# Kernel tuning notes

Measured on AMD Instinct MI355X. Metric: run time of the kernel, lower is better.

The kernel has to match this reference:

```python
import jax, jax.numpy as jnp
import numpy as np

N_HEADS = 16  # emb_dim 512 // head_dim 32


def _heads(t, h=N_HEADS):
    b, n, d = t.shape
    return t.reshape(b, n, h, d // h).transpose(0, 2, 1, 3)  # [b h n hd]


def _merge(t):
    b, h, n, hd = t.shape
    return t.transpose(0, 2, 1, 3).reshape(b, n, h * hd)


def setup_inputs() -> dict:
    key = jax.random.key(0)
    ks = jax.random.split(key, 6)
    b, n, nc, d = 2, 2048, 256, 512
    x = jax.random.normal(ks[0], (b, n, d), dtype=jnp.float32)
    clusters = jax.random.normal(ks[1], (b, nc, d), dtype=jnp.float32)
    token_sizes = jax.random.uniform(ks[2], (b, n), dtype=jnp.float32)
    Wq = jax.random.normal(ks[3], (d, d), dtype=jnp.float32) * 0.02
    Wkv = jax.random.normal(ks[4], (d, 2 * d), dtype=jnp.float32) * 0.02
    Wo = jax.random.normal(ks[5], (d, d), dtype=jnp.float32) * 0.02
    return {"x": x, "clusters": clusters, "token_sizes": token_sizes,
            "Wq": Wq, "Wkv": Wkv, "Wo": Wo}


def reference(x, clusters, token_sizes, Wq, Wkv, Wo):
    b, n, d = x.shape
    hd = d // N_HEADS
    scale = hd ** -0.5

    q_in = jnp.concatenate([x, clusters], axis=1)       # pack tokens + clusters as queries
    q = _heads(q_in @ Wq)                               # [b h n+nc hd]
    kv = x @ Wkv                                        # [b n 2d]
    k = _heads(kv[..., :d])                             # [b h n hd]
    v = _heads(kv[..., d:])                             # [b h n hd]

    attn = jnp.einsum('bhqd,bhkd->bhqk', q, k) * scale  # [b h n+nc n]
    attn_x = attn[:, :, :n, :]                          # token queries  [b h n n]
    attn_c = attn[:, :, n:, :]                          # cluster queries [b h nc n]

    # soft assignment: softmax over cluster axis, then row-normalize
    a_c = jax.nn.softmax(attn_c, axis=-2)
    a_c = a_c / (jnp.sum(a_c, axis=-1, keepdims=True) + 1e-5)
    clusters_out = _merge(jnp.einsum('bhck,bhkd->bhcd', a_c, v)) @ Wo  # [b nc d]

    # additive log token-size bias on the query axis (as in the original)
    attn_x = attn_x + jnp.log(token_sizes + 1e-10)[:, None, :, None]
    a_x = jax.nn.softmax(attn_x, axis=-1)
    x_out = _merge(jnp.einsum('bhqk,bhkd->bhqd', a_x, v)) @ Wo  # [b n d]

    return x_out, clusters_out
```

## Files before the change

kernel.cpp:

```cpp
#include <hip/hip_runtime.h>
#include <hip/hip_bf16.h>

#define N_TOK 2048
#define N_CLU 256
#define N_ALL 2304
#define DMODEL 512
#define NH 16
#define HD 32
#define BATCH 2
#define SCALE 0.17677669529663687f

typedef short bf16x8 __attribute__((ext_vector_type(8)));
typedef float f32x4  __attribute__((ext_vector_type(4)));
typedef unsigned short u16;

static __device__ __forceinline__ u16 f2b(float x) {
    __hip_bfloat16 h = __float2bfloat16(x);
    return *reinterpret_cast<u16*>(&h);
}
static __device__ __forceinline__ unsigned int cvt_pk_bf16(float lo, float hi) {
    unsigned int r;
    asm("v_cvt_pk_bf16_f32 %0, %1, %2" : "=v"(r) : "v"(lo), "v"(hi));
    return r;
}
static __device__ __forceinline__ void async16(u16* lds, const u16* g) {
    __builtin_amdgcn_global_load_lds(
        (const __attribute__((address_space(1))) unsigned int*)g,
        (__attribute__((address_space(3))) unsigned int*)lds, 16, 0, 0);
}

__global__ __launch_bounds__(256) void cvt_bf16_k(const float* __restrict__ in,
                                                  u16* __restrict__ out)
{
    const long i = ((long)blockIdx.x * 256 + threadIdx.x) * 8;
    float4 a = *(const float4*)(in + i);
    float4 b = *(const float4*)(in + i + 4);
    u16 v[8] = { f2b(a.x), f2b(a.y), f2b(a.z), f2b(a.w),
                 f2b(b.x), f2b(b.y), f2b(b.z), f2b(b.w) };
    *(bf16x8*)(out + i) = *(const bf16x8*)v;
}

__global__ __launch_bounds__(256) void cvtT_k(const float* __restrict__ W,
                                              u16* __restrict__ WT,
                                              int R, int C, float scale)
{
    __shared__ float tile[32][33];
    const int tx = threadIdx.x & 31, ty = threadIdx.x >> 5;
    const int c0 = blockIdx.x * 32, r0 = blockIdx.y * 32;
    #pragma unroll
    for (int i = 0; i < 4; i++)
        tile[ty + i * 8][tx] = W[(long)(r0 + ty + i * 8) * C + c0 + tx];
    __syncthreads();
    #pragma unroll
    for (int i = 0; i < 4; i++)
        WT[(long)(c0 + ty + i * 8) * R + r0 + tx] = f2b(tile[tx][ty + i * 8] * scale);
}

__global__ __launch_bounds__(256) void gemm_bf16(
    const u16* __restrict__ A, long sA,
    const u16* __restrict__ BT,
    void* __restrict__ Cv, long sC,
    int N, int K, int out_fp32)
{
    const int t = threadIdx.x;
    const int m0 = blockIdx.y * 128, n0 = blockIdx.x * 128;
    A += (long)blockIdx.z * sA;
    __shared__ u16 As[128 * 32];
    __shared__ u16 Bs[128 * 32];
    const int wid = t >> 6, lane = t & 63;
    const int lr = lane & 15, lg = lane >> 4;
    const int wr = wid >> 1, wc = wid & 1;
    f32x4 acc[4][4] = {};
    const int o1 = t * 16, o2 = o1 + 4096;
    const int row1 = o1 >> 6, ke1 = (o1 & 63) >> 1;
    const int row2 = o2 >> 6, ke2 = (o2 & 63) >> 1;
    for (int k0 = 0; k0 < K; k0 += 32) {
        async16(As + (o1 >> 1), A  + (long)(m0 + row1) * K + k0 + ke1);
        async16(As + (o2 >> 1), A  + (long)(m0 + row2) * K + k0 + ke2);
        async16(Bs + (o1 >> 1), BT + (long)(n0 + row1) * K + k0 + ke1);
        async16(Bs + (o2 >> 1), BT + (long)(n0 + row2) * K + k0 + ke2);
        __syncthreads();
        bf16x8 af[4], bfr[4];
        #pragma unroll
        for (int i = 0; i < 4; i++) {
            af[i]  = *(const bf16x8*)&As[(wr * 64 + i * 16 + lr) * 32 + lg * 8];
            bfr[i] = *(const bf16x8*)&Bs[(wc * 64 + i * 16 + lr) * 32 + lg * 8];
        }
        #pragma unroll
        for (int mi = 0; mi < 4; mi++)
            #pragma unroll
            for (int ni = 0; ni < 4; ni++)
                acc[mi][ni] = __builtin_amdgcn_mfma_f32_16x16x32_bf16(af[mi], bfr[ni], acc[mi][ni], 0, 0, 0);
        __syncthreads();
    }
    if (out_fp32) {
        float* C = (float*)Cv + (long)blockIdx.z * sC;
        #pragma unroll
        for (int mi = 0; mi < 4; mi++)
            #pragma unroll
            for (int ni = 0; ni < 4; ni++) {
                const long rbase = m0 + wr * 64 + mi * 16 + lg * 4;
                #pragma unroll
                for (int r = 0; r < 4; r++)
                    C[(rbase + r) * N + n0 + wc * 64 + ni * 16 + lr] = acc[mi][ni][r];
            }
    } else {
        u16* C = (u16*)Cv + (long)blockIdx.z * sC;
        #pragma unroll
        for (int mi = 0; mi < 4; mi++)
            #pragma unroll
            for (int ni = 0; ni < 4; ni++) {
                const long rbase = m0 + wr * 64 + mi * 16 + lg * 4;
                #pragma unroll
                for (int r = 0; r < 4; r++)
                    C[(rbase + r) * N + n0 + wc * 64 + ni * 16 + lr] = f2b(acc[mi][ni][r]);
            }
    }
}

__global__ __launch_bounds__(256) void vt_prep(
    const u16* __restrict__ kvb, u16* __restrict__ vt)
{
    const int b = blockIdx.z, h = blockIdx.y, k0 = blockIdx.x * 64;
    const int t = threadIdx.x;
    __shared__ u16 tile[64][48];
    {
        const int key = t >> 2, dc = (t & 3) * 8;
        *(bf16x8*)&tile[key][dc] = *(const bf16x8*)(
            kvb + ((long)b * N_TOK + k0 + key) * (2 * DMODEL) + DMODEL + h * HD + dc);
    }
    __syncthreads();
    {
        const int d = t & 31, kc = (t >> 5) * 8;
        bf16x8 v;
        #pragma unroll
        for (int i = 0; i < 8; i++) v[i] = (short)tile[kc + i][d];
        *(bf16x8*)(vt + (((long)(b * NH + h)) * HD + d) * N_TOK + k0 + kc) = v;
    }
}

__global__ __launch_bounds__(256) void attn_x2(
    const u16* __restrict__ qb, const u16* __restrict__ kvb,
    const u16* __restrict__ vt, u16* __restrict__ aob)
{
    const int b = blockIdx.z, h = blockIdx.y;
    const int wid = threadIdx.x >> 6, lane = threadIdx.x & 63;
    const int lr = lane & 15, lg = lane >> 4;
    const int q0 = blockIdx.x * 128 + wid * 32;

    __shared__ unsigned int Pl[4][32][36];
    unsigned int (*P)[36] = Pl[wid];

    bf16x8 qf[2];
    #pragma unroll
    for (int qs = 0; qs < 2; qs++)
        qf[qs] = *(const bf16x8*)(qb + ((long)b * N_ALL + q0 + qs * 16 + lr) * DMODEL + h * HD + lg * 8);

    f32x4 o[2][2] = {};
    float rs[2] = {0.f, 0.f};
    const u16* kbase = kvb + (long)b * N_TOK * (2 * DMODEL) + h * HD + lg * 8;
    const u16* vbase = vt + ((long)(b * NH + h)) * HD * N_TOK;

    for (int k0 = 0; k0 < N_TOK; k0 += 64) {
        bf16x8 kf[4];
        #pragma unroll
        for (int kg = 0; kg < 4; kg++)
            kf[kg] = *(const bf16x8*)(kbase + (long)(k0 + kg * 16 + lr) * (2 * DMODEL));
        #pragma unroll
        for (int qs = 0; qs < 2; qs++) {
            #pragma unroll
            for (int kg = 0; kg < 4; kg++) {
                f32x4 z = {0.f, 0.f, 0.f, 0.f};
                f32x4 s = __builtin_amdgcn_mfma_f32_16x16x32_bf16(kf[kg], qf[qs], z, 0, 0, 0);
                float e0 = __expf(s[0]), e1 = __expf(s[1]);
                float e2 = __expf(s[2]), e3 = __expf(s[3]);
                rs[qs] += (e0 + e1) + (e2 + e3);
                uint2 w = { cvt_pk_bf16(e0, e1), cvt_pk_bf16(e2, e3) };
                *(uint2*)&P[qs * 16 + lr][kg * 8 + lg * 2] = w;
            }
        }
        #pragma unroll
        for (int c = 0; c < 2; c++) {
            bf16x8 pb0 = *(const bf16x8*)&P[lr][c * 16 + lg * 4];
            bf16x8 pb1 = *(const bf16x8*)&P[16 + lr][c * 16 + lg * 4];
            #pragma unroll
            for (int dg = 0; dg < 2; dg++) {
                bf16x8 vf = *(const bf16x8*)(vbase + (long)(dg * 16 + lr) * N_TOK + k0 + c * 32 + lg * 8);
                o[0][dg] = __builtin_amdgcn_mfma_f32_16x16x32_bf16(vf, pb0, o[0][dg], 0, 0, 0);
                o[1][dg] = __builtin_amdgcn_mfma_f32_16x16x32_bf16(vf, pb1, o[1][dg], 0, 0, 0);
            }
        }
    }
    float inv[2];
    #pragma unroll
    for (int qs = 0; qs < 2; qs++) {
        float v = rs[qs];
        v += __shfl_xor(v, 16);
        v += __shfl_xor(v, 32);
        inv[qs] = 1.f / v;
    }
    u16* Ow = (u16*)P;
    #pragma unroll
    for (int qs = 0; qs < 2; qs++)
        #pragma unroll
        for (int dg = 0; dg < 2; dg++)
            #pragma unroll
            for (int r = 0; r < 4; r++)
                Ow[(qs * 16 + lr) * 72 + dg * 16 + lg * 4 + r] = f2b(o[qs][dg][r] * inv[qs]);
    const int rrow = lane >> 2, seg = lane & 3;
    #pragma unroll
    for (int rep = 0; rep < 2; rep++) {
        bf16x8 v = *(const bf16x8*)&Ow[(rep * 16 + rrow) * 72 + seg * 8];
        *(bf16x8*)(aob + ((long)b * N_ALL + q0 + rep * 16 + rrow) * DMODEL + h * HD + seg * 8) = v;
    }
}

__global__ __launch_bounds__(256) void attn_c_mfma(
    const u16* __restrict__ qb, const u16* __restrict__ kvb,
    const u16* __restrict__ vt, float* __restrict__ part)
{
    const int b = blockIdx.z, h = blockIdx.y, kblk = blockIdx.x;
    const int wid = threadIdx.x >> 6, lane = threadIdx.x & 63;
    const int lr = lane & 15, lg = lane >> 4;
    const int c0 = wid * 64;

    __shared__ u16 Pl[4][64][72];
    __shared__ float cs2[64][4];
    u16 (*P)[72] = Pl[wid];

    bf16x8 qf[4];
    #pragma unroll
    for (int qs = 0; qs < 4; qs++)
        qf[qs] = *(const bf16x8*)(
            qb + ((long)b * N_ALL + N_TOK + c0 + qs * 16 + lr) * DMODEL + h * HD + lg * 8);

    f32x4 o[4][2] = {};
    float rs[4][4] = {};
    const u16* kbase = kvb + (long)b * N_TOK * (2 * DMODEL) + h * HD + lg * 8;
    const u16* vbase = vt + ((long)(b * NH + h)) * HD * N_TOK;

    for (int kt = 0; kt < 4; kt++) {
        const int k0 = kblk * 256 + kt * 64;
        bf16x8 kf[4];
        #pragma unroll
        for (int kg = 0; kg < 4; kg++)
            kf[kg] = *(const bf16x8*)(kbase + (long)(k0 + kg * 16 + lr) * (2 * DMODEL));
        f32x4 e[4][4];
        #pragma unroll
        for (int qs = 0; qs < 4; qs++)
            #pragma unroll
            for (int kg = 0; kg < 4; kg++) {
                f32x4 z = {0.f, 0.f, 0.f, 0.f};
                e[qs][kg] = __builtin_amdgcn_mfma_f32_16x16x32_bf16(qf[qs], kf[kg], z, 0, 0, 0);
            }
        float csum[4];
        #pragma unroll
        for (int kg = 0; kg < 4; kg++) {
            float v = 0.f;
            #pragma unroll
            for (int qs = 0; qs < 4; qs++)
                #pragma unroll
                for (int r = 0; r < 4; r++) {
                    float p = __expf(e[qs][kg][r]);
                    e[qs][kg][r] = p;
                    v += p;
                }
            v += __shfl_xor(v, 16);
            v += __shfl_xor(v, 32);
            csum[kg] = v;
        }
        float own = (lg == 0) ? csum[0] : (lg == 1) ? csum[1] : (lg == 2) ? csum[2] : csum[3];
        __syncthreads();
        cs2[lane][wid] = own;
        __syncthreads();
        float ics0, ics1, ics2, ics3;
        {
            f32x4 c4;
            c4 = *(const f32x4*)&cs2[ 0 + lr][0]; ics0 = 1.f / (c4[0] + c4[1] + c4[2] + c4[3]);
            c4 = *(const f32x4*)&cs2[16 + lr][0]; ics1 = 1.f / (c4[0] + c4[1] + c4[2] + c4[3]);
            c4 = *(const f32x4*)&cs2[32 + lr][0]; ics2 = 1.f / (c4[0] + c4[1] + c4[2] + c4[3]);
            c4 = *(const f32x4*)&cs2[48 + lr][0]; ics3 = 1.f / (c4[0] + c4[1] + c4[2] + c4[3]);
        }
        #pragma unroll
        for (int qs = 0; qs < 4; qs++)
            #pragma unroll
            for (int kg = 0; kg < 4; kg++) {
                const float ics = (kg == 0) ? ics0 : (kg == 1) ? ics1 : (kg == 2) ? ics2 : ics3;
                #pragma unroll
                for (int r = 0; r < 4; r++) {
                    float p = e[qs][kg][r] * ics;
                    rs[qs][r] += p;
                    P[qs * 16 + lg * 4 + r][kg * 16 + lr] = f2b(p);
                }
            }
        #pragma unroll
        for (int kh = 0; kh < 2; kh++) {
            bf16x8 pf[4];
            #pragma unroll
            for (int qs = 0; qs < 4; qs++)
                pf[qs] = *(const bf16x8*)&P[qs * 16 + lr][kh * 32 + lg * 8];
            #pragma unroll
            for (int dg = 0; dg < 2; dg++) {
                bf16x8 vf = *(const bf16x8*)(
                    vbase + (long)(dg * 16 + lr) * N_TOK + k0 + kh * 32 + lg * 8);
                #pragma unroll
                for (int qs = 0; qs < 4; qs++)
                    o[qs][dg] = __builtin_amdgcn_mfma_f32_16x16x32_bf16(pf[qs], vf, o[qs][dg], 0, 0, 0);
            }
        }
    }
    float* pp = part + ((((long)(b * NH + h)) * 8 + kblk) * 256) * 36;
    #pragma unroll
    for (int qs = 0; qs < 4; qs++)
        #pragma unroll
        for (int r = 0; r < 4; r++) {
            const int row = c0 + qs * 16 + lg * 4 + r;
            pp[(long)row * 36 + lr]      = o[qs][0][r];
            pp[(long)row * 36 + 16 + lr] = o[qs][1][r];
            float v = rs[qs][r];
            v += __shfl_xor(v, 1); v += __shfl_xor(v, 2);
            v += __shfl_xor(v, 4); v += __shfl_xor(v, 8);
            if (lr == 0) pp[(long)row * 36 + 32] = v;
        }
}

__global__ __launch_bounds__(256) void attn_c_reduce(
    const float* __restrict__ part, u16* __restrict__ aob)
{
    const int gid = blockIdx.x * 256 + threadIdx.x;
    const int b = gid >> 12, h = (gid >> 8) & 15, c = gid & 255;
    float acc[32] = {};
    float rsum = 0.f;
    for (int j = 0; j < 8; j++) {
        const float* pp = part + ((((long)(b * NH + h)) * 8 + j) * 256 + c) * 36;
        #pragma unroll
        for (int e4 = 0; e4 < 8; e4++) {
            f32x4 v = *(const f32x4*)(pp + e4 * 4);
            acc[e4 * 4 + 0] += v[0]; acc[e4 * 4 + 1] += v[1];
            acc[e4 * 4 + 2] += v[2]; acc[e4 * 4 + 3] += v[3];
        }
        rsum += pp[32];
    }
    const float inv = 1.f / (rsum + 1e-5f);
    u16* orow = aob + ((long)b * N_ALL + N_TOK + c) * DMODEL + h * HD;
    #pragma unroll
    for (int e = 0; e < 32; e++) orow[e] = f2b(acc[e] * inv);
}

extern "C" void kernel_launch(void* const* d_in, const int* in_sizes, int n_in,
                              void* d_out, int out_size, void* d_ws, size_t ws_size,
                              hipStream_t stream)
{
    const float* x        = (const float*)d_in[0];
    const float* clusters = (const float*)d_in[1];
    const float* Wq  = (const float*)d_in[3];
    const float* Wkv = (const float*)d_in[4];
    const float* Wo  = (const float*)d_in[5];
    float* out = (float*)d_out;

    char* ws = (char*)d_ws;
    u16*   xb   = (u16*)(ws);
    u16*   cb   = (u16*)(ws + 4194304);
    u16*   WqT  = (u16*)(ws + 4718592);
    u16*   WkvT = (u16*)(ws + 5242880);
    u16*   WoT  = (u16*)(ws + 6291456);
    u16*   qb   = (u16*)(ws + 6815744);
    u16*   kvb  = (u16*)(ws + 11534336);
    u16*   vt   = (u16*)(ws + 19922944);
    u16*   aob  = (u16*)(ws + 24117248);
    float* part = (float*)(ws + 28835840);

    cvt_bf16_k<<<dim3(1024), 256, 0, stream>>>(x, xb);
    cvt_bf16_k<<<dim3(128),  256, 0, stream>>>(clusters, cb);
    cvtT_k<<<dim3(16, 16), 256, 0, stream>>>(Wq,  WqT,  512,  512, SCALE);
    cvtT_k<<<dim3(32, 16), 256, 0, stream>>>(Wkv, WkvT, 512, 1024, 1.f);
    cvtT_k<<<dim3(16, 16), 256, 0, stream>>>(Wo,  WoT,  512,  512, 1.f);

    gemm_bf16<<<dim3(4, 16, 2), 256, 0, stream>>>(
        xb, (long)N_TOK * DMODEL, WqT, qb, (long)N_ALL * DMODEL, DMODEL, DMODEL, 0);
    gemm_bf16<<<dim3(4, 2, 2), 256, 0, stream>>>(
        cb, (long)N_CLU * DMODEL, WqT, qb + (long)N_TOK * DMODEL, (long)N_ALL * DMODEL, DMODEL, DMODEL, 0);
    gemm_bf16<<<dim3(8, 16, 2), 256, 0, stream>>>(
        xb, (long)N_TOK * DMODEL, WkvT, kvb, (long)N_TOK * 2 * DMODEL, 2 * DMODEL, DMODEL, 0);

    vt_prep<<<dim3(32, 16, 2), 256, 0, stream>>>(kvb, vt);

    attn_x2<<<dim3(16, 16, 2), 256, 0, stream>>>(qb, kvb, vt, aob);
    attn_c_mfma<<<dim3(8, 16, 2), 256, 0, stream>>>(qb, kvb, vt, part);
    attn_c_reduce<<<dim3(32), 256, 0, stream>>>(part, aob);

    gemm_bf16<<<dim3(4, 16, 2), 256, 0, stream>>>(
        aob, (long)N_ALL * DMODEL, WoT, out, (long)N_TOK * DMODEL, DMODEL, DMODEL, 1);
    gemm_bf16<<<dim3(4, 2, 2), 256, 0, stream>>>(
        aob + (long)N_TOK * DMODEL, (long)N_ALL * DMODEL, WoT,
        out + (long)BATCH * N_TOK * DMODEL, (long)N_CLU * DMODEL, DMODEL, DMODEL, 1);
}
```

Before: 252.3 us.

## Fuse QKV projection, split-K token attention, exp2 scaling, merged output GEMM

Concatenates Wq and Wkv into one weight so a single GEMM produces Q, K and V for tokens, with the cluster queries going to a separate buffer. It folds log2(e) into the Q scale so the softmax can use a hardware exp2, and swizzles the P tile in LDS to cut bank conflicts. The token-attention kernel now runs 8 waves per block, each half covering half the keys, and combines the partial results through LDS. The two output-projection GEMMs become one launch that remaps rows into the token and cluster outputs. Fewer launches and more parallelism per block are traded for extra LDS use and a cross-wave combine step.

```diff
diff --git a/kernel.cpp b/kernel.cpp
--- a/kernel.cpp
+++ b/kernel.cpp
@@ -8,7 +8,7 @@
 #define NH 16
 #define HD 32
 #define BATCH 2
-#define SCALE 0.17677669529663687f
+#define EXPSCALE 0.25503486f
 
 typedef short bf16x8 __attribute__((ext_vector_type(8)));
 typedef float f32x4  __attribute__((ext_vector_type(4)));
@@ -23,6 +23,11 @@
     asm("v_cvt_pk_bf16_f32 %0, %1, %2" : "=v"(r) : "v"(lo), "v"(hi));
     return r;
 }
+#if __has_builtin(__builtin_amdgcn_exp2f)
+#define EXP2(x) __builtin_amdgcn_exp2f(x)
+#else
+#define EXP2(x) exp2f(x)
+#endif
 static __device__ __forceinline__ void async16(u16* lds, const u16* g) {
     __builtin_amdgcn_global_load_lds(
         (const __attribute__((address_space(1))) unsigned int*)g,
@@ -60,7 +65,7 @@
     const u16* __restrict__ A, long sA,
     const u16* __restrict__ BT,
     void* __restrict__ Cv, long sC,
-    int N, int K, int out_fp32)
+    int N, int K, int mode)
 {
     const int t = threadIdx.x;
     const int m0 = blockIdx.y * 128, n0 = blockIdx.x * 128;
@@ -93,8 +98,25 @@
                 acc[mi][ni] = __builtin_amdgcn_mfma_f32_16x16x32_bf16(af[mi], bfr[ni], acc[mi][ni], 0, 0, 0);
         __syncthreads();
     }
-    if (out_fp32) {
-        float* C = (float*)Cv + (long)blockIdx.z * sC;
+    if (mode == 1) {
+        float* C = (float*)Cv;
+        #pragma unroll
+        for (int mi = 0; mi < 4; mi++)
+            #pragma unroll
+            for (int ni = 0; ni < 4; ni++) {
+                const int rbase = m0 + wr * 64 + mi * 16 + lg * 4;
+                #pragma unroll
+                for (int r = 0; r < 4; r++) {
+                    int rw = rbase + r;
+                    int bb = rw >= N_ALL;
+                    int w  = rw - bb * N_ALL;
+                    long orow = (w < N_TOK) ? ((long)bb * N_TOK + w)
+                                            : (2L * N_TOK + (long)bb * N_CLU + (w - N_TOK));
+                    C[orow * N + n0 + wc * 64 + ni * 16 + lr] = acc[mi][ni][r];
+                }
+            }
+    } else {
+        u16* C = (u16*)Cv + (long)blockIdx.z * sC;
         #pragma unroll
         for (int mi = 0; mi < 4; mi++)
             #pragma unroll
@@ -102,24 +124,13 @@
                 const long rbase = m0 + wr * 64 + mi * 16 + lg * 4;
                 #pragma unroll
                 for (int r = 0; r < 4; r++)
-                    C[(rbase + r) * N + n0 + wc * 64 + ni * 16 + lr] = acc[mi][ni][r];
-            }
-    } else {
-        u16* C = (u16*)Cv + (long)blockIdx.z * sC;
-        #pragma unroll
-        for (int mi = 0; mi < 4; mi++)
-            #pragma unroll
-            for (int ni = 0; ni < 4; ni++) {
-                const long rbase = m0 + wr * 64 + mi * 16 + lg * 4;
-                #pragma unroll
-                for (int r = 0; r < 4; r++)
                     C[(rbase + r) * N + n0 + wc * 64 + ni * 16 + lr] = f2b(acc[mi][ni][r]);
             }
     }
 }
 
 __global__ __launch_bounds__(256) void vt_prep(
-    const u16* __restrict__ kvb, u16* __restrict__ vt)
+    const u16* __restrict__ qkv, u16* __restrict__ vt)
 {
     const int b = blockIdx.z, h = blockIdx.y, k0 = blockIdx.x * 64;
     const int t = threadIdx.x;
@@ -127,7 +138,7 @@
     {
         const int key = t >> 2, dc = (t & 3) * 8;
         *(bf16x8*)&tile[key][dc] = *(const bf16x8*)(
-            kvb + ((long)b * N_TOK + k0 + key) * (2 * DMODEL) + DMODEL + h * HD + dc);
+            qkv + ((long)b * N_TOK + k0 + key) * 1536 + 1024 + h * HD + dc);
     }
     __syncthreads();
     {
@@ -139,84 +150,114 @@
     }
 }
 
-__global__ __launch_bounds__(256) void attn_x2(
-    const u16* __restrict__ qb, const u16* __restrict__ kvb,
-    const u16* __restrict__ vt, u16* __restrict__ aob)
+__global__ __launch_bounds__(512) void attn_x3(
+    const u16* __restrict__ qkv, const u16* __restrict__ vt,
+    u16* __restrict__ aob)
 {
     const int b = blockIdx.z, h = blockIdx.y;
     const int wid = threadIdx.x >> 6, lane = threadIdx.x & 63;
     const int lr = lane & 15, lg = lane >> 4;
-    const int q0 = blockIdx.x * 128 + wid * 32;
-
-    __shared__ unsigned int Pl[4][32][36];
-    unsigned int (*P)[36] = Pl[wid];
+    const int q0 = blockIdx.x * 128 + (wid & 3) * 32;
+    const int khalf = wid >> 2;
+
+    __shared__ unsigned int P[8][32][32];
+    __shared__ float comb[4][64][18];
+    __shared__ u16 Ot[4][32][40];
+
+    unsigned int (*Pw)[32] = P[wid];
+    const int sw = 4 * (lr & 7);
 
     bf16x8 qf[2];
     #pragma unroll
     for (int qs = 0; qs < 2; qs++)
-        qf[qs] = *(const bf16x8*)(qb + ((long)b * N_ALL + q0 + qs * 16 + lr) * DMODEL + h * HD + lg * 8);
+        qf[qs] = *(const bf16x8*)(
+            qkv + ((long)b * N_TOK + q0 + qs * 16 + lr) * 1536 + h * HD + lg * 8);
 
     f32x4 o[2][2] = {};
     float rs[2] = {0.f, 0.f};
-    const u16* kbase = kvb + (long)b * N_TOK * (2 * DMODEL) + h * HD + lg * 8;
+    const u16* kbase = qkv + (long)b * N_TOK * 1536 + 512 + h * HD + lg * 8;
     const u16* vbase = vt + ((long)(b * NH + h)) * HD * N_TOK;
 
-    for (int k0 = 0; k0 < N_TOK; k0 += 64) {
+    const int kend = khalf * 1024 + 1024;
+    for (int k0 = khalf * 1024; k0 < kend; k0 += 64) {
         bf16x8 kf[4];
         #pragma unroll
         for (int kg = 0; kg < 4; kg++)
-            kf[kg] = *(const bf16x8*)(kbase + (long)(k0 + kg * 16 + lr) * (2 * DMODEL));
+            kf[kg] = *(const bf16x8*)(kbase + (long)(k0 + kg * 16 + lr) * 1536);
         #pragma unroll
         for (int qs = 0; qs < 2; qs++) {
             #pragma unroll
             for (int kg = 0; kg < 4; kg++) {
                 f32x4 z = {0.f, 0.f, 0.f, 0.f};
                 f32x4 s = __builtin_amdgcn_mfma_f32_16x16x32_bf16(kf[kg], qf[qs], z, 0, 0, 0);
-                float e0 = __expf(s[0]), e1 = __expf(s[1]);
-                float e2 = __expf(s[2]), e3 = __expf(s[3]);
+                float e0 = EXP2(s[0]), e1 = EXP2(s[1]);
+                float e2 = EXP2(s[2]), e3 = EXP2(s[3]);
                 rs[qs] += (e0 + e1) + (e2 + e3);
                 uint2 w = { cvt_pk_bf16(e0, e1), cvt_pk_bf16(e2, e3) };
-                *(uint2*)&P[qs * 16 + lr][kg * 8 + lg * 2] = w;
+                *(uint2*)&Pw[qs * 16 + lr][(kg * 8 + lg * 2) ^ sw] = w;
             }
         }
         #pragma unroll
         for (int c = 0; c < 2; c++) {
-            bf16x8 pb0 = *(const bf16x8*)&P[lr][c * 16 + lg * 4];
-            bf16x8 pb1 = *(const bf16x8*)&P[16 + lr][c * 16 + lg * 4];
+            bf16x8 pb0 = *(const bf16x8*)&Pw[lr][(c * 16 + lg * 4) ^ sw];
+            bf16x8 pb1 = *(const bf16x8*)&Pw[16 + lr][(c * 16 + lg * 4) ^ sw];
             #pragma unroll
             for (int dg = 0; dg < 2; dg++) {
-                bf16x8 vf = *(const bf16x8*)(vbase + (long)(dg * 16 + lr) * N_TOK + k0 + c * 32 + lg * 8);
+                bf16x8 vf = *(const bf16x8*)(
+                    vbase + (long)(dg * 16 + lr) * N_TOK + k0 + c * 32 + lg * 8);
                 o[0][dg] = __builtin_amdgcn_mfma_f32_16x16x32_bf16(vf, pb0, o[0][dg], 0, 0, 0);
                 o[1][dg] = __builtin_amdgcn_mfma_f32_16x16x32_bf16(vf, pb1, o[1][dg], 0, 0, 0);
             }
         }
     }
-    float inv[2];
     #pragma unroll
     for (int qs = 0; qs < 2; qs++) {
-        float v = rs[qs];
-        v += __shfl_xor(v, 16);
-        v += __shfl_xor(v, 32);
-        inv[qs] = 1.f / v;
-    }
-    u16* Ow = (u16*)P;
-    #pragma unroll
-    for (int qs = 0; qs < 2; qs++)
+        rs[qs] += __shfl_xor(rs[qs], 16);
+        rs[qs] += __shfl_xor(rs[qs], 32);
+    }
+    if (wid >= 4) {
+        float* cp = &comb[wid - 4][lane][0];
+        #pragma unroll
+        for (int qs = 0; qs < 2; qs++)
+            #pragma unroll
+            for (int dg = 0; dg < 2; dg++)
+                #pragma unroll
+                for (int r = 0; r < 4; r++)
+                    cp[qs * 8 + dg * 4 + r] = o[qs][dg][r];
+        cp[16] = rs[0];
+        cp[17] = rs[1];
+    }
+    __syncthreads();
+    if (wid < 4) {
+        const float* cp = &comb[wid][lane][0];
+        #pragma unroll
+        for (int qs = 0; qs < 2; qs++)
+            #pragma unroll
+            for (int dg = 0; dg < 2; dg++)
+                #pragma unroll
+                for (int r = 0; r < 4; r++)
+                    o[qs][dg][r] += cp[qs * 8 + dg * 4 + r];
+        rs[0] += cp[16];
+        rs[1] += cp[17];
+        const float inv0 = 1.f / rs[0], inv1 = 1.f / rs[1];
         #pragma unroll
         for (int dg = 0; dg < 2; dg++)
             #pragma unroll
-            for (int r = 0; r < 4; r++)
-                Ow[(qs * 16 + lr) * 72 + dg * 16 + lg * 4 + r] = f2b(o[qs][dg][r] * inv[qs]);
-    const int rrow = lane >> 2, seg = lane & 3;
-    #pragma unroll
-    for (int rep = 0; rep < 2; rep++) {
-        bf16x8 v = *(const bf16x8*)&Ow[(rep * 16 + rrow) * 72 + seg * 8];
-        *(bf16x8*)(aob + ((long)b * N_ALL + q0 + rep * 16 + rrow) * DMODEL + h * HD + seg * 8) = v;
+            for (int r = 0; r < 4; r++) {
+                Ot[wid][lr][dg * 16 + lg * 4 + r]      = f2b(o[0][dg][r] * inv0);
+                Ot[wid][16 + lr][dg * 16 + lg * 4 + r] = f2b(o[1][dg][r] * inv1);
+            }
+        const int rrow = lane >> 2, seg = lane & 3;
+        #pragma unroll
+        for (int rep = 0; rep < 2; rep++) {
+            bf16x8 v = *(const bf16x8*)&Ot[wid][rep * 16 + rrow][seg * 8];
+            *(bf16x8*)(aob + ((long)b * N_ALL + q0 + rep * 16 + rrow) * DMODEL + h * HD + seg * 8) = v;
+        }
     }
 }
 
 __global__ __launch_bounds__(256) void attn_c_mfma(
-    const u16* __restrict__ qb, const u16* __restrict__ kvb,
+    const u16* __restrict__ qc, const u16* __restrict__ qkv,
     const u16* __restrict__ vt, float* __restrict__ part)
 {
     const int b = blockIdx.z, h = blockIdx.y, kblk = blockIdx.x;
@@ -232,11 +273,11 @@
     #pragma unroll
     for (int qs = 0; qs < 4; qs++)
         qf[qs] = *(const bf16x8*)(
-            qb + ((long)b * N_ALL + N_TOK + c0 + qs * 16 + lr) * DMODEL + h * HD + lg * 8);
+            qc + ((long)(b * N_CLU) + c0 + qs * 16 + lr) * DMODEL + h * HD + lg * 8);
 
     f32x4 o[4][2] = {};
     float rs[4][4] = {};
-    const u16* kbase = kvb + (long)b * N_TOK * (2 * DMODEL) + h * HD + lg * 8;
+    const u16* kbase = qkv + (long)b * N_TOK * 1536 + 512 + h * HD + lg * 8;
     const u16* vbase = vt + ((long)(b * NH + h)) * HD * N_TOK;
 
     for (int kt = 0; kt < 4; kt++) {
@@ -244,7 +285,7 @@
         bf16x8 kf[4];
         #pragma unroll
         for (int kg = 0; kg < 4; kg++)
-            kf[kg] = *(const bf16x8*)(kbase + (long)(k0 + kg * 16 + lr) * (2 * DMODEL));
+            kf[kg] = *(const bf16x8*)(kbase + (long)(k0 + kg * 16 + lr) * 1536);
         f32x4 e[4][4];
         #pragma unroll
         for (int qs = 0; qs < 4; qs++)
@@ -261,7 +302,7 @@
             for (int qs = 0; qs < 4; qs++)
                 #pragma unroll
                 for (int r = 0; r < 4; r++) {
-                    float p = __expf(e[qs][kg][r]);
+                    float p = EXP2(e[qs][kg][r]);
                     e[qs][kg][r] = p;
                     v += p;
                 }
@@ -359,39 +400,33 @@
     float* out = (float*)d_out;
 
     char* ws = (char*)d_ws;
-    u16*   xb   = (u16*)(ws);
-    u16*   cb   = (u16*)(ws + 4194304);
-    u16*   WqT  = (u16*)(ws + 4718592);
-    u16*   WkvT = (u16*)(ws + 5242880);
-    u16*   WoT  = (u16*)(ws + 6291456);
-    u16*   qb   = (u16*)(ws + 6815744);
-    u16*   kvb  = (u16*)(ws + 11534336);
-    u16*   vt   = (u16*)(ws + 19922944);
-    u16*   aob  = (u16*)(ws + 24117248);
-    float* part = (float*)(ws + 28835840);
+    u16*   xb    = (u16*)(ws);
+    u16*   cb    = (u16*)(ws + 4194304);
+    u16*   WcatT = (u16*)(ws + 4718592);
+    u16*   WoT   = (u16*)(ws + 6291456);
+    u16*   qkv   = (u16*)(ws + 6815744);
+    u16*   qc    = (u16*)(ws + 19398656);
+    u16*   vt    = (u16*)(ws + 19922944);
+    u16*   aob   = (u16*)(ws + 24117248);
+    float* part  = (float*)(ws + 28835840);
 
     cvt_bf16_k<<<dim3(1024), 256, 0, stream>>>(x, xb);
     cvt_bf16_k<<<dim3(128),  256, 0, stream>>>(clusters, cb);
-    cvtT_k<<<dim3(16, 16), 256, 0, stream>>>(Wq,  WqT,  512,  512, SCALE);
-    cvtT_k<<<dim3(32, 16), 256, 0, stream>>>(Wkv, WkvT, 512, 1024, 1.f);
-    cvtT_k<<<dim3(16, 16), 256, 0, stream>>>(Wo,  WoT,  512,  512, 1.f);
-
-    gemm_bf16<<<dim3(4, 16, 2), 256, 0, stream>>>(
-        xb, (long)N_TOK * DMODEL, WqT, qb, (long)N_ALL * DMODEL, DMODEL, DMODEL, 0);
+    cvtT_k<<<dim3(16, 16), 256, 0, stream>>>(Wq,  WcatT,             512,  512, EXPSCALE);
+    cvtT_k<<<dim3(32, 16), 256, 0, stream>>>(Wkv, WcatT + 512 * 512, 512, 1024, 1.f);
+    cvtT_k<<<dim3(16, 16), 256, 0, stream>>>(Wo,  WoT,               512,  512, 1.f);
+
+    gemm_bf16<<<dim3(12, 16, 2), 256, 0, stream>>>(
+        xb, (long)N_TOK * DMODEL, WcatT, qkv, (long)N_TOK * 1536, 1536, DMODEL, 0);
     gemm_bf16<<<dim3(4, 2, 2), 256, 0, stream>>>(
-        cb, (long)N_CLU * DMODEL, WqT, qb + (long)N_TOK * DMODEL, (long)N_ALL * DMODEL, DMODEL, DMODEL, 0);
-    gemm_bf16<<<dim3(8, 16, 2), 256, 0, stream>>>(
-        xb, (long)N_TOK * DMODEL, WkvT, kvb, (long)N_TOK * 2 * DMODEL, 2 * DMODEL, DMODEL, 0);
-
-    vt_prep<<<dim3(32, 16, 2), 256, 0, stream>>>(kvb, vt);
-
-    attn_x2<<<dim3(16, 16, 2), 256, 0, stream>>>(qb, kvb, vt, aob);
-    attn_c_mfma<<<dim3(8, 16, 2), 256, 0, stream>>>(qb, kvb, vt, part);
+        cb, (long)N_CLU * DMODEL, WcatT, qc, (long)N_CLU * DMODEL, DMODEL, DMODEL, 0);
+
+    vt_prep<<<dim3(32, 16, 2), 256, 0, stream>>>(qkv, vt);
+
+    attn_x3<<<dim3(16, 16, 2), 512, 0, stream>>>(qkv, vt, aob);
+    attn_c_mfma<<<dim3(8, 16, 2), 256, 0, stream>>>(qc, qkv, vt, part);
     attn_c_reduce<<<dim3(32), 256, 0, stream>>>(part, aob);
 
-    gemm_bf16<<<dim3(4, 16, 2), 256, 0, stream>>>(
-        aob, (long)N_ALL * DMODEL, WoT, out, (long)N_TOK * DMODEL, DMODEL, DMODEL, 1);
-    gemm_bf16<<<dim3(4, 2, 2), 256, 0, stream>>>(
-        aob + (long)N_TOK * DMODEL, (long)N_ALL * DMODEL, WoT,
-        out + (long)BATCH * N_TOK * DMODEL, (long)N_CLU * DMODEL, DMODEL, DMODEL, 1);
-}
+    gemm_bf16<<<dim3(4, 36, 1), 256, 0, stream>>>(
+        aob, 0, WoT, out, 0, DMODEL, DMODEL, 1);
+}
```

Result: faster. 221.5 us (-12.2%).
